# Kernel tuning notes

Hardware: AMD Instinct MI355X
Metric: run time of the kernel (lower is better)

## Reference

```python
import jax, jax.numpy as jnp
import numpy as np

D_MODEL = 1024
N_HEAD = 16
D_HEAD = D_MODEL // N_HEAD


def setup_inputs() -> dict:
    key = jax.random.key(0)
    k_x, k_qkv, k_proj = jax.random.split(key, 3)
    B, T = 2, 2048
    x = jax.random.normal(k_x, (B, T, D_MODEL), dtype=jnp.float32)
    # torch Linear weight [out, in]; y = x @ W.T. Scale ~ kaiming-uniform-ish.
    s = 1.0 / np.sqrt(D_MODEL)
    W_qkv = jax.random.uniform(k_qkv, (3 * D_MODEL, D_MODEL), dtype=jnp.float32, minval=-s, maxval=s)
    W_proj = jax.random.uniform(k_proj, (D_MODEL, D_MODEL), dtype=jnp.float32, minval=-s, maxval=s)
    return {"x": x, "W_qkv": W_qkv, "W_proj": W_proj}


def reference(x, W_qkv, W_proj):
    B, T, C = x.shape
    qkv = jnp.einsum('btc,oc->bto', x, W_qkv)  # [B,T,3C]
    q, k, v = jnp.split(qkv, 3, axis=-1)
    # [B,T,C] -> [B,H,T,Dh]
    def heads(t):
        return t.reshape(B, T, N_HEAD, D_HEAD).transpose(0, 2, 1, 3)
    q, k, v = heads(q), heads(k), heads(v)
    scale = 1.0 / np.sqrt(D_HEAD)
    scores = jnp.einsum('bhqd,bhkd->bhqk', q, k) * scale  # [B,H,T,T]
    causal = jnp.tril(jnp.ones((T, T), dtype=bool))
    scores = jnp.where(causal, scores, jnp.finfo(scores.dtype).min)
    attn = jax.nn.softmax(scores, axis=-1)
    y = jnp.einsum('bhqk,bhkd->bhqd', attn, v)  # [B,H,T,Dh]
    y = y.transpose(0, 2, 1, 3).reshape(B, T, C)
    return jnp.einsum('btc,oc->bto', y, W_proj)
```

## Files before the change

### kernel.cpp

```cpp
#include <hip/hip_runtime.h>

typedef unsigned short u16;
typedef float f32x4 __attribute__((ext_vector_type(4)));
typedef __bf16 bf16x8 __attribute__((ext_vector_type(8)));
typedef unsigned int u32x4 __attribute__((ext_vector_type(4)));
typedef u16 u16x4 __attribute__((ext_vector_type(4)));
typedef u16 u16x8 __attribute__((ext_vector_type(8)));

static __device__ __forceinline__ u16 f2bf(float f) {
  union { __bf16 h; u16 u; } c;
  c.h = (__bf16)f;
  return c.u;
}
static __device__ __forceinline__ float bf2f(u16 u) {
  union { unsigned u; float f; } c;
  c.u = ((unsigned)u) << 16;
  return c.f;
}

static __device__ __forceinline__ void gload_lds16(const void* g, void* l) {
  __builtin_amdgcn_global_load_lds(
      (const __attribute__((address_space(1))) unsigned int*)g,
      (__attribute__((address_space(3))) unsigned int*)l, 16, 0, 0);
}

__global__ __launch_bounds__(256) void cvt3_f32_bf16(const float* __restrict__ a,
                                                     const float* __restrict__ bb,
                                                     const float* __restrict__ cc,
                                                     u16* __restrict__ out,
                                                     int n1, int n2, int n3) {
  int i = blockIdx.x * 256 + threadIdx.x;
  const float* src;
  int j = i;
  if (i < n1) { src = a; }
  else if (i < n1 + n2) { src = bb; j = i - n1; }
  else { src = cc; j = i - n1 - n2; if (j >= n3) return; }
  f32x4 v = *((const f32x4*)src + j);
  u16x4 o;
  o[0] = f2bf(v[0]); o[1] = f2bf(v[1]); o[2] = f2bf(v[2]); o[3] = f2bf(v[3]);
  *((u16x4*)out + i) = o;
}

template<int OUT_BF16, int FUSE_VT>
__global__ __launch_bounds__(256) void gemm_nt(const u16* __restrict__ A,
                                               const u16* __restrict__ B,
                                               void* __restrict__ Cp,
                                               u16* __restrict__ vt,
                                               int M, int N, int K, int gy) {
  __shared__ __align__(16) u16 lA[128 * 64];
  __shared__ __align__(16) u16 lB[128 * 64];
  const int tid = threadIdx.x;
  const int lane = tid & 63;
  const int wave = tid >> 6;
  const int wm = wave >> 1, wn = wave & 1;
  const int l15 = lane & 15, lg = lane >> 4;

  const int bid = blockIdx.x;
  const int xcd = bid & 7, s = bid >> 3;
  const int pnx = (N >> 7) >> 3;
  const int bm = (s % gy) * 128;
  const int bn = (xcd * pnx + s / gy) * 128;

  f32x4 acc[4][4];
#pragma unroll
  for (int i = 0; i < 4; ++i)
#pragma unroll
    for (int j = 0; j < 4; ++j) acc[i][j] = (f32x4){0.f, 0.f, 0.f, 0.f};

  const u16* Ag[4];
  const u16* Bg[4];
#pragma unroll
  for (int it = 0; it < 4; ++it) {
    const int ss = it * 256 + tid;
    const int row = ss >> 3, g = ss & 7;
    const int gsw = g ^ (row & 7);
    Ag[it] = A + (size_t)(bm + row) * K + gsw * 8;
    Bg[it] = B + (size_t)(bn + row) * K + gsw * 8;
  }

  for (int k0 = 0; k0 < K; k0 += 64) {
#pragma unroll
    for (int it = 0; it < 4; ++it) {
      gload_lds16(Ag[it] + k0, (u16*)lA + (size_t)(it * 256 + tid) * 8);
      gload_lds16(Bg[it] + k0, (u16*)lB + (size_t)(it * 256 + tid) * 8);
    }
    __syncthreads();
#pragma unroll
    for (int kk = 0; kk < 2; ++kk) {
      bf16x8 af[4], bfv[4];
#pragma unroll
      for (int mf = 0; mf < 4; ++mf) {
        const int row = wm * 64 + mf * 16 + l15;
        af[mf] = *(const bf16x8*)((const char*)lA + row * 128 +
                                  ((kk * 64 + lg * 16) ^ ((row & 7) << 4)));
      }
#pragma unroll
      for (int nf = 0; nf < 4; ++nf) {
        const int row = wn * 64 + nf * 16 + l15;
        bfv[nf] = *(const bf16x8*)((const char*)lB + row * 128 +
                                   ((kk * 64 + lg * 16) ^ ((row & 7) << 4)));
      }
#pragma unroll
      for (int mf = 0; mf < 4; ++mf)
#pragma unroll
        for (int nf = 0; nf < 4; ++nf)
          acc[mf][nf] = __builtin_amdgcn_mfma_f32_16x16x32_bf16(af[mf], bfv[nf], acc[mf][nf], 0, 0, 0);
    }
    __syncthreads();
  }

  if (FUSE_VT && bn >= 2048) {
#pragma unroll
    for (int mf = 0; mf < 4; ++mf) {
      const int row0 = bm + wm * 64 + mf * 16 + lg * 4;
      const int b = row0 >> 11, t0 = row0 & 2047;
#pragma unroll
      for (int nf = 0; nf < 4; ++nf) {
        const int colv = bn - 2048 + wn * 64 + nf * 16 + l15;
        const int h = colv >> 6, d = colv & 63;
        u16x4 pk;
        pk[0] = f2bf(acc[mf][nf][0]); pk[1] = f2bf(acc[mf][nf][1]);
        pk[2] = f2bf(acc[mf][nf][2]); pk[3] = f2bf(acc[mf][nf][3]);
        *(u16x4*)&vt[((size_t)((b * 16 + h) * 64 + d)) * 2048 + t0] = pk;
      }
    }
  } else {
#pragma unroll
    for (int mf = 0; mf < 4; ++mf) {
#pragma unroll
      for (int r = 0; r < 4; ++r) {
        const int row = bm + wm * 64 + mf * 16 + lg * 4 + r;
#pragma unroll
        for (int nf = 0; nf < 4; ++nf) {
          const int col = bn + wn * 64 + nf * 16 + l15;
          const float v = acc[mf][nf][r];
          if (OUT_BF16) ((u16*)Cp)[(size_t)row * N + col] = f2bf(v);
          else          ((float*)Cp)[(size_t)row * N + col] = v;
        }
      }
    }
  }
}

__global__ __launch_bounds__(512) void attn_fwd(const u16* __restrict__ qkv,
                                                const u16* __restrict__ vt,
                                                u16* __restrict__ po,
                                                float* __restrict__ mlf) {
  constexpr int T = 2048, C = 1024, C3 = 3072, D = 64;
  __shared__ __align__(16) u16 lK[2][64 * 64];
  __shared__ __align__(16) u16 lV[2][64 * 64];
  __shared__ __align__(16) u16 lP[8 * 16 * 64];
  const int tid = threadIdx.x, lane = tid & 63, w = tid >> 6;
  const int l15 = lane & 15, lg = lane >> 4;

  const int bid = blockIdx.x;
  const int xcd = bid & 7, slot = bid >> 3;
  const int bh = xcd * 4 + (slot >> 4);
  const int rem = slot & 15;
  const int pi = rem >> 1, hf = rem & 1;
  const int b = bh >> 4, h = bh & 15;

  const int r0 = tid >> 3, off0 = (tid & 7) * 8;
  const int sb0 = (off0 * 2) ^ ((r0 & 7) << 4);
  const u16* Kbase = qkv + (size_t)b * T * C3 + C + h * D;
  const u16* Vbase = vt + (size_t)bh * D * T;
  char* lPb = (char*)lP + w * 2048;

  const float qscale = 0.125f * 1.44269504088896f;

#pragma unroll 1
  for (int qi = 0; qi < 2; ++qi) {
    const int qt = (qi == 0) ? pi : (15 - pi);
    const int q0 = qt * 128;
    const int kts = hf ? (qt + 1) : 0;
    const int kte = hf ? (2 * qt + 2) : (qt + 1);
    const int nit = kte - kts;
    const int qrow = q0 + w * 16 + l15;

    const size_t qoff = ((size_t)b * T + qrow) * C3 + h * D;
    const bf16x8 aq0 = *(const bf16x8*)&qkv[qoff + lg * 8];
    const bf16x8 aq1 = *(const bf16x8*)&qkv[qoff + 32 + lg * 8];

    float m = -1.0e30f, l = 0.f;
    f32x4 o_acc[4];
#pragma unroll
    for (int nf = 0; nf < 4; ++nf) o_acc[nf] = (f32x4){0.f, 0.f, 0.f, 0.f};

    u32x4 rk0 = *(const u32x4*)(Kbase + (size_t)(kts * 64 + r0) * C3 + off0);
    u32x4 rv0 = *(const u32x4*)(Vbase + (size_t)r0 * T + kts * 64 + off0);
    __syncthreads();
    *(u32x4*)&lK[0][(r0 * 128 + sb0) >> 1] = rk0;
    *(u32x4*)&lV[0][(r0 * 128 + sb0) >> 1] = rv0;
    if (nit > 1) {
      rk0 = *(const u32x4*)(Kbase + (size_t)((kts + 1) * 64 + r0) * C3 + off0);
      rv0 = *(const u32x4*)(Vbase + (size_t)r0 * T + (kts + 1) * 64 + off0);
    }

    for (int i = 0; i < nit; ++i) {
      const int kt = kts + i;
      const int cur = i & 1;
      __syncthreads();
      if (i < nit - 1) {
        *(u32x4*)&lK[cur ^ 1][(r0 * 128 + sb0) >> 1] = rk0;
        *(u32x4*)&lV[cur ^ 1][(r0 * 128 + sb0) >> 1] = rv0;
        if (i + 1 < nit - 1) {
          const int kn = (kt + 2) * 64;
          rk0 = *(const u32x4*)(Kbase + (size_t)(kn + r0) * C3 + off0);
          rv0 = *(const u32x4*)(Vbase + (size_t)r0 * T + kn + off0);
        }
      }
      const u16* Kc = lK[cur];
      const u16* Vc = lV[cur];

      f32x4 s[4];
#pragma unroll
      for (int nf = 0; nf < 4; ++nf) s[nf] = (f32x4){0.f, 0.f, 0.f, 0.f};
      __builtin_amdgcn_s_setprio(1);
#pragma unroll
      for (int nf = 0; nf < 4; ++nf) {
        const int row = nf * 16 + l15;
        const int x = (row & 7) << 4;
        bf16x8 bk0 = *(const bf16x8*)&Kc[(row * 128 + ((lg * 16) ^ x)) >> 1];
        bf16x8 bk1 = *(const bf16x8*)&Kc[(row * 128 + ((64 + lg * 16) ^ x)) >> 1];
        s[nf] = __builtin_amdgcn_mfma_f32_16x16x32_bf16(bk0, aq0, s[nf], 0, 0, 0);
        s[nf] = __builtin_amdgcn_mfma_f32_16x16x32_bf16(bk1, aq1, s[nf], 0, 0, 0);
      }
      __builtin_amdgcn_s_setprio(0);

      if (kt >= 2 * qt) {
        const int kb = kt * 64;
#pragma unroll
        for (int nf = 0; nf < 4; ++nf)
#pragma unroll
          for (int r = 0; r < 4; ++r) {
            float v = s[nf][r] * qscale;
            if (kb + nf * 16 + lg * 4 + r > qrow) v = -1.0e30f;
            s[nf][r] = v;
          }
      } else {
#pragma unroll
        for (int nf = 0; nf < 4; ++nf)
#pragma unroll
          for (int r = 0; r < 4; ++r) s[nf][r] *= qscale;
      }

      float t0a = fmaxf(fmaxf(s[0][0], s[0][1]), fmaxf(s[0][2], s[0][3]));
      float t1a = fmaxf(fmaxf(s[1][0], s[1][1]), fmaxf(s[1][2], s[1][3]));
      float t2a = fmaxf(fmaxf(s[2][0], s[2][1]), fmaxf(s[2][2], s[2][3]));
      float t3a = fmaxf(fmaxf(s[3][0], s[3][1]), fmaxf(s[3][2], s[3][3]));
      float pmax = fmaxf(fmaxf(t0a, t1a), fmaxf(t2a, t3a));
      pmax = fmaxf(pmax, __shfl_xor(pmax, 16));
      pmax = fmaxf(pmax, __shfl_xor(pmax, 32));

      if (!__all(pmax <= m)) {
        const float mnew = fmaxf(m, pmax);
        const float fct = __builtin_amdgcn_exp2f(m - mnew);
        m = mnew;
        l *= fct;
#pragma unroll
        for (int r = 0; r < 4; ++r) {
          const float fr = __shfl(fct, lg * 4 + r);
#pragma unroll
          for (int nf = 0; nf < 4; ++nf) o_acc[nf][r] *= fr;
        }
      }

      float p[4][4];
#pragma unroll
      for (int nf = 0; nf < 4; ++nf)
#pragma unroll
        for (int r = 0; r < 4; ++r) p[nf][r] = __builtin_amdgcn_exp2f(s[nf][r] - m);
      float s0a = (p[0][0] + p[0][1]) + (p[0][2] + p[0][3]);
      float s1a = (p[1][0] + p[1][1]) + (p[1][2] + p[1][3]);
      float s2a = (p[2][0] + p[2][1]) + (p[2][2] + p[2][3]);
      float s3a = (p[3][0] + p[3][1]) + (p[3][2] + p[3][3]);
      float psum = (s0a + s1a) + (s2a + s3a);
      psum += __shfl_xor(psum, 16);
      psum += __shfl_xor(psum, 32);
      l += psum;

#pragma unroll
      for (int nf = 0; nf < 4; ++nf) {
        u16x4 pk;
        pk[0] = f2bf(p[nf][0]); pk[1] = f2bf(p[nf][1]);
        pk[2] = f2bf(p[nf][2]); pk[3] = f2bf(p[nf][3]);
        *(u16x4*)(lPb + l15 * 128 + ((nf * 32 + lg * 8) ^ ((l15 & 7) << 4))) = pk;
      }

      __builtin_amdgcn_s_setprio(1);
#pragma unroll
      for (int sj = 0; sj < 2; ++sj) {
        bf16x8 ap = *(const bf16x8*)(lPb + l15 * 128 + ((sj * 64 + lg * 16) ^ ((l15 & 7) << 4)));
#pragma unroll
        for (int nf = 0; nf < 4; ++nf) {
          const int d = nf * 16 + l15;
          bf16x8 bv = *(const bf16x8*)&Vc[(d * 128 + ((sj * 64 + lg * 16) ^ ((d & 7) << 4))) >> 1];
          o_acc[nf] = __builtin_amdgcn_mfma_f32_16x16x32_bf16(ap, bv, o_acc[nf], 0, 0, 0);
        }
      }
      __builtin_amdgcn_s_setprio(0);
    }

    u16* pob = po + (size_t)hf * (4096ull * 1024ull);
#pragma unroll
    for (int r = 0; r < 4; ++r) {
      const float lv = __shfl(l, lg * 4 + r);
      const float li = (lv > 0.f) ? __builtin_amdgcn_rcpf(lv) : 0.f;
      const int row = q0 + w * 16 + lg * 4 + r;
#pragma unroll
      for (int nf = 0; nf < 4; ++nf) {
        const int col = h * D + nf * 16 + l15;
        pob[((size_t)b * T + row) * C + col] = f2bf(o_acc[nf][r] * li);
      }
    }
    if (lg == 0) {
      const size_t idx = (size_t)(b * T + qrow) * 16 + h;
      float* mp = mlf + (size_t)hf * 131072ull + idx * 2;
      mp[0] = m;
      mp[1] = l;
    }
  }
}

__global__ __launch_bounds__(256) void merge_o(const u16* __restrict__ po,
                                               const float* __restrict__ mlf,
                                               u16* __restrict__ y) {
  const int gid = blockIdx.x * 256 + threadIdx.x;
  const int row = gid >> 3, d0 = (gid & 7) * 8;
  const int bt = row >> 4, h = row & 15;
  const float m1 = mlf[row * 2], l1 = mlf[row * 2 + 1];
  const float m2 = mlf[131072 + row * 2], l2 = mlf[131072 + row * 2 + 1];
  const float ms = fmaxf(m1, m2);
  const float a1 = l1 * __builtin_amdgcn_exp2f(m1 - ms);
  const float a2 = l2 * __builtin_amdgcn_exp2f(m2 - ms);
  const float inv = __builtin_amdgcn_rcpf(a1 + a2);
  const float w1 = a1 * inv, w2 = a2 * inv;
  const size_t off = (size_t)bt * 1024 + h * 64 + d0;
  u16x8 p1 = *(const u16x8*)&po[off];
  u16x8 p2 = *(const u16x8*)&po[4194304ull + off];
  u16x8 o;
#pragma unroll
  for (int j = 0; j < 8; ++j) o[j] = f2bf(w1 * bf2f(p1[j]) + w2 * bf2f(p2[j]));
  *(u16x8*)&y[off] = o;
}

extern "C" void kernel_launch(void* const* d_in, const int* in_sizes, int n_in,
                              void* d_out, int out_size, void* d_ws, size_t ws_size,
                              hipStream_t stream) {
  const float* x = (const float*)d_in[0];
  const float* Wqkv = (const float*)d_in[1];
  const float* Wproj = (const float*)d_in[2];
  float* out = (float*)d_out;

  constexpr int B = 2, T = 2048, C = 1024, C3 = 3072, H = 16, D = 64;
  constexpr int M = B * T;

  u16* xb = (u16*)d_ws;
  u16* wqkvb = xb + (size_t)M * C;
  u16* wprojb = wqkvb + (size_t)C3 * C;
  u16* qkvb = wprojb + (size_t)C * C;
  u16* vtb = qkvb + (size_t)M * C3;
  u16* yb = vtb + (size_t)M * C;
  u16* po = yb + (size_t)M * C;
  float* mlf = (float*)(po + 2ull * M * C);

  constexpr int n1 = (M * C) / 4, n2 = (C3 * C) / 4, n3 = (C * C) / 4;
  cvt3_f32_bf16<<<dim3((n1 + n2 + n3 + 255) / 256), 256, 0, stream>>>(
      x, Wqkv, Wproj, xb, n1, n2, n3);

  gemm_nt<1, 1><<<dim3((C3 / 128) * (M / 128)), 256, 0, stream>>>(
      xb, wqkvb, qkvb, vtb, M, C3, C, M / 128);
  attn_fwd<<<dim3(512), 512, 0, stream>>>(qkvb, vtb, po, mlf);
  merge_o<<<dim3(2048), 256, 0, stream>>>(po, mlf, yb);
  gemm_nt<0, 0><<<dim3((C / 128) * (M / 128)), 256, 0, stream>>>(
      yb, wprojb, out, nullptr, M, C, C, M / 128);
}
```

Before: 110.8 us.

## Switch attention to 32x32 MFMA with register-resident P and three-way KV split

The attention kernel now uses 4 waves of 32 query rows each with 32x32x16 bf16 MFMA, keeping the softmax probabilities in registers. It packs them with v_cvt_pk_bf16_f32 and v_permlane32_swap instead of round-tripping P through LDS. The KV range is split three ways across 768 blocks instead of two, and a three-way merge kernel combines the partials, with the third partial buffer reusing the x bf16 workspace. Output is staged through LDS for 16-byte coalesced stores. The aim is to cut LDS traffic and shuffles and improve load balance and occupancy, at the cost of an extra partial buffer to write and read in the merge.

After: 266.2 us. +140.2%, slower.

```diff
diff --git a/kernel.cpp b/kernel.cpp
--- a/kernel.cpp
+++ b/kernel.cpp
@@ -2,6 +2,7 @@
 
 typedef unsigned short u16;
 typedef float f32x4 __attribute__((ext_vector_type(4)));
+typedef float f32x16 __attribute__((ext_vector_type(16)));
 typedef __bf16 bf16x8 __attribute__((ext_vector_type(8)));
 typedef unsigned int u32x4 __attribute__((ext_vector_type(4)));
 typedef u16 u16x4 __attribute__((ext_vector_type(4)));
@@ -16,6 +17,14 @@
   union { unsigned u; float f; } c;
   c.u = ((unsigned)u) << 16;
   return c.f;
+}
+static __device__ __forceinline__ unsigned cvtpk(float a, float b) {
+  unsigned r;
+  asm volatile("v_cvt_pk_bf16_f32 %0, %1, %2" : "=v"(r) : "v"(a), "v"(b));
+  return r;
+}
+static __device__ __forceinline__ void plswap(unsigned& a, unsigned& b) {
+  asm volatile("v_permlane32_swap_b32 %0, %1" : "+v"(a), "+v"(b));
 }
 
 static __device__ __forceinline__ void gload_lds16(const void* g, void* l) {
@@ -142,29 +151,32 @@
   }
 }
 
-__global__ __launch_bounds__(512) void attn_fwd(const u16* __restrict__ qkv,
-                                                const u16* __restrict__ vt,
-                                                u16* __restrict__ po,
-                                                float* __restrict__ mlf) {
-  constexpr int T = 2048, C = 1024, C3 = 3072, D = 64;
+__global__ __launch_bounds__(256, 3) void attn_fwd(const u16* __restrict__ qkv,
+                                                   const u16* __restrict__ vt,
+                                                   u16* __restrict__ po0,
+                                                   u16* __restrict__ po1,
+                                                   u16* __restrict__ po2,
+                                                   float* __restrict__ mlf) {
+  constexpr int T = 2048, C3 = 3072;
   __shared__ __align__(16) u16 lK[2][64 * 64];
   __shared__ __align__(16) u16 lV[2][64 * 64];
-  __shared__ __align__(16) u16 lP[8 * 16 * 64];
   const int tid = threadIdx.x, lane = tid & 63, w = tid >> 6;
-  const int l15 = lane & 15, lg = lane >> 4;
+  const int l31 = lane & 31, h5 = lane >> 5;
 
   const int bid = blockIdx.x;
   const int xcd = bid & 7, slot = bid >> 3;
-  const int bh = xcd * 4 + (slot >> 4);
-  const int rem = slot & 15;
-  const int pi = rem >> 1, hf = rem & 1;
+  const int bh = xcd * 4 + slot / 24;
+  const int rem = slot % 24;
+  const int pi = rem / 3, tr = rem % 3;
   const int b = bh >> 4, h = bh & 15;
 
   const int r0 = tid >> 3, off0 = (tid & 7) * 8;
+  const int r1 = r0 + 32;
   const int sb0 = (off0 * 2) ^ ((r0 & 7) << 4);
-  const u16* Kbase = qkv + (size_t)b * T * C3 + C + h * D;
-  const u16* Vbase = vt + (size_t)bh * D * T;
-  char* lPb = (char*)lP + w * 2048;
+  const int sb1 = (off0 * 2) ^ ((r1 & 7) << 4);
+  const u16* Kbase = qkv + (size_t)b * T * C3 + 1024 + h * 64;
+  const u16* Vbase = vt + (size_t)bh * 64 * T;
+  u16* pob = (tr == 0) ? po0 : ((tr == 1) ? po1 : po2);
 
   const float qscale = 0.125f * 1.44269504088896f;
 
@@ -172,175 +184,216 @@
   for (int qi = 0; qi < 2; ++qi) {
     const int qt = (qi == 0) ? pi : (15 - pi);
     const int q0 = qt * 128;
-    const int kts = hf ? (qt + 1) : 0;
-    const int kte = hf ? (2 * qt + 2) : (qt + 1);
+    const int n = 2 * qt + 2;
+    const int kts = tr * n / 3, kte = (tr + 1) * n / 3;
     const int nit = kte - kts;
-    const int qrow = q0 + w * 16 + l15;
-
-    const size_t qoff = ((size_t)b * T + qrow) * C3 + h * D;
-    const bf16x8 aq0 = *(const bf16x8*)&qkv[qoff + lg * 8];
-    const bf16x8 aq1 = *(const bf16x8*)&qkv[qoff + 32 + lg * 8];
+    const int qrow = q0 + w * 32 + l31;
+
+    const size_t qoff = ((size_t)b * T + qrow) * C3 + h * 64;
+    bf16x8 aq[4];
+#pragma unroll
+    for (int ks = 0; ks < 4; ++ks)
+      aq[ks] = *(const bf16x8*)&qkv[qoff + ks * 16 + h5 * 8];
 
     float m = -1.0e30f, l = 0.f;
-    f32x4 o_acc[4];
-#pragma unroll
-    for (int nf = 0; nf < 4; ++nf) o_acc[nf] = (f32x4){0.f, 0.f, 0.f, 0.f};
-
-    u32x4 rk0 = *(const u32x4*)(Kbase + (size_t)(kts * 64 + r0) * C3 + off0);
-    u32x4 rv0 = *(const u32x4*)(Vbase + (size_t)r0 * T + kts * 64 + off0);
+    f32x16 o0, o1;
+#pragma unroll
+    for (int r = 0; r < 16; ++r) { o0[r] = 0.f; o1[r] = 0.f; }
+
+    if (nit > 0) {
+      u32x4 rk0 = *(const u32x4*)(Kbase + (size_t)(kts * 64 + r0) * C3 + off0);
+      u32x4 rk1 = *(const u32x4*)(Kbase + (size_t)(kts * 64 + r1) * C3 + off0);
+      u32x4 rv0 = *(const u32x4*)(Vbase + (size_t)r0 * T + kts * 64 + off0);
+      u32x4 rv1 = *(const u32x4*)(Vbase + (size_t)r1 * T + kts * 64 + off0);
+      __syncthreads();
+      *(u32x4*)((char*)lK[0] + r0 * 128 + sb0) = rk0;
+      *(u32x4*)((char*)lK[0] + r1 * 128 + sb1) = rk1;
+      *(u32x4*)((char*)lV[0] + r0 * 128 + sb0) = rv0;
+      *(u32x4*)((char*)lV[0] + r1 * 128 + sb1) = rv1;
+      if (nit > 1) {
+        rk0 = *(const u32x4*)(Kbase + (size_t)((kts + 1) * 64 + r0) * C3 + off0);
+        rk1 = *(const u32x4*)(Kbase + (size_t)((kts + 1) * 64 + r1) * C3 + off0);
+        rv0 = *(const u32x4*)(Vbase + (size_t)r0 * T + (kts + 1) * 64 + off0);
+        rv1 = *(const u32x4*)(Vbase + (size_t)r1 * T + (kts + 1) * 64 + off0);
+      }
+
+      for (int i = 0; i < nit; ++i) {
+        const int kt = kts + i;
+        const int cur = i & 1;
+        __syncthreads();
+        if (i < nit - 1) {
+          *(u32x4*)((char*)lK[cur ^ 1] + r0 * 128 + sb0) = rk0;
+          *(u32x4*)((char*)lK[cur ^ 1] + r1 * 128 + sb1) = rk1;
+          *(u32x4*)((char*)lV[cur ^ 1] + r0 * 128 + sb0) = rv0;
+          *(u32x4*)((char*)lV[cur ^ 1] + r1 * 128 + sb1) = rv1;
+          if (i + 1 < nit - 1) {
+            const int kn = (kt + 2) * 64;
+            rk0 = *(const u32x4*)(Kbase + (size_t)(kn + r0) * C3 + off0);
+            rk1 = *(const u32x4*)(Kbase + (size_t)(kn + r1) * C3 + off0);
+            rv0 = *(const u32x4*)(Vbase + (size_t)r0 * T + kn + off0);
+            rv1 = *(const u32x4*)(Vbase + (size_t)r1 * T + kn + off0);
+          }
+        }
+        const char* Kc = (const char*)lK[cur];
+        const char* Vc = (const char*)lV[cur];
+
+        f32x16 s0, s1;
+#pragma unroll
+        for (int r = 0; r < 16; ++r) { s0[r] = 0.f; s1[r] = 0.f; }
+        __builtin_amdgcn_s_setprio(1);
+#pragma unroll
+        for (int ks = 0; ks < 4; ++ks) {
+          const int cb = (ks * 32 + h5 * 16);
+          bf16x8 kf0 = *(const bf16x8*)(Kc + l31 * 128 + (cb ^ ((l31 & 7) << 4)));
+          bf16x8 kf1 = *(const bf16x8*)(Kc + (32 + l31) * 128 + (cb ^ ((l31 & 7) << 4)));
+          s0 = __builtin_amdgcn_mfma_f32_32x32x16_bf16(kf0, aq[ks], s0, 0, 0, 0);
+          s1 = __builtin_amdgcn_mfma_f32_32x32x16_bf16(kf1, aq[ks], s1, 0, 0, 0);
+        }
+        __builtin_amdgcn_s_setprio(0);
+
+        if (kt >= 2 * qt) {
+          const int kb0 = kt * 64;
+#pragma unroll
+          for (int r = 0; r < 16; ++r) {
+            const int kvl = (r & 3) + 8 * (r >> 2) + 4 * h5;
+            float v0 = s0[r] * qscale;
+            float v1 = s1[r] * qscale;
+            if (kb0 + kvl > qrow) v0 = -1.0e30f;
+            if (kb0 + 32 + kvl > qrow) v1 = -1.0e30f;
+            s0[r] = v0; s1[r] = v1;
+          }
+        } else {
+#pragma unroll
+          for (int r = 0; r < 16; ++r) { s0[r] *= qscale; s1[r] *= qscale; }
+        }
+
+        float t0 = fmaxf(fmaxf(s0[0], s0[1]), fmaxf(s0[2], s0[3]));
+        float t1 = fmaxf(fmaxf(s0[4], s0[5]), fmaxf(s0[6], s0[7]));
+        float t2 = fmaxf(fmaxf(s0[8], s0[9]), fmaxf(s0[10], s0[11]));
+        float t3 = fmaxf(fmaxf(s0[12], s0[13]), fmaxf(s0[14], s0[15]));
+        float t4 = fmaxf(fmaxf(s1[0], s1[1]), fmaxf(s1[2], s1[3]));
+        float t5 = fmaxf(fmaxf(s1[4], s1[5]), fmaxf(s1[6], s1[7]));
+        float t6 = fmaxf(fmaxf(s1[8], s1[9]), fmaxf(s1[10], s1[11]));
+        float t7 = fmaxf(fmaxf(s1[12], s1[13]), fmaxf(s1[14], s1[15]));
+        float pmax = fmaxf(fmaxf(fmaxf(t0, t1), fmaxf(t2, t3)),
+                           fmaxf(fmaxf(t4, t5), fmaxf(t6, t7)));
+        pmax = fmaxf(pmax, __shfl_xor(pmax, 32));
+
+        if (!__all(pmax <= m)) {
+          const float mnew = fmaxf(m, pmax);
+          const float fct = __builtin_amdgcn_exp2f(m - mnew);
+          m = mnew;
+          l *= fct;
+#pragma unroll
+          for (int r = 0; r < 16; ++r) { o0[r] *= fct; o1[r] *= fct; }
+        }
+
+#pragma unroll
+        for (int r = 0; r < 16; ++r) {
+          s0[r] = __builtin_amdgcn_exp2f(s0[r] - m);
+          s1[r] = __builtin_amdgcn_exp2f(s1[r] - m);
+        }
+        float u0 = (s0[0] + s0[1]) + (s0[2] + s0[3]);
+        float u1 = (s0[4] + s0[5]) + (s0[6] + s0[7]);
+        float u2 = (s0[8] + s0[9]) + (s0[10] + s0[11]);
+        float u3 = (s0[12] + s0[13]) + (s0[14] + s0[15]);
+        float u4 = (s1[0] + s1[1]) + (s1[2] + s1[3]);
+        float u5 = (s1[4] + s1[5]) + (s1[6] + s1[7]);
+        float u6 = (s1[8] + s1[9]) + (s1[10] + s1[11]);
+        float u7 = (s1[12] + s1[13]) + (s1[14] + s1[15]);
+        float psum = ((u0 + u1) + (u2 + u3)) + ((u4 + u5) + (u6 + u7));
+        psum += __shfl_xor(psum, 32);
+        l += psum;
+
+        union { u32x4 u; bf16x8 b; } pb[4];
+        {
+          unsigned A = cvtpk(s0[0], s0[1]), Bw = cvtpk(s0[2], s0[3]);
+          unsigned Cw = cvtpk(s0[4], s0[5]), Dw = cvtpk(s0[6], s0[7]);
+          unsigned E = cvtpk(s0[8], s0[9]), F = cvtpk(s0[10], s0[11]);
+          unsigned G = cvtpk(s0[12], s0[13]), H = cvtpk(s0[14], s0[15]);
+          plswap(A, Cw); plswap(Bw, Dw); plswap(E, G); plswap(F, H);
+          pb[0].u = (u32x4){A, Bw, Cw, Dw};
+          pb[1].u = (u32x4){E, F, G, H};
+        }
+        {
+          unsigned A = cvtpk(s1[0], s1[1]), Bw = cvtpk(s1[2], s1[3]);
+          unsigned Cw = cvtpk(s1[4], s1[5]), Dw = cvtpk(s1[6], s1[7]);
+          unsigned E = cvtpk(s1[8], s1[9]), F = cvtpk(s1[10], s1[11]);
+          unsigned G = cvtpk(s1[12], s1[13]), H = cvtpk(s1[14], s1[15]);
+          plswap(A, Cw); plswap(Bw, Dw); plswap(E, G); plswap(F, H);
+          pb[2].u = (u32x4){A, Bw, Cw, Dw};
+          pb[3].u = (u32x4){E, F, G, H};
+        }
+
+        __builtin_amdgcn_s_setprio(1);
+#pragma unroll
+        for (int kk = 0; kk < 4; ++kk) {
+          const int cb = (kk * 32 + h5 * 16);
+          bf16x8 vf0 = *(const bf16x8*)(Vc + l31 * 128 + (cb ^ ((l31 & 7) << 4)));
+          bf16x8 vf1 = *(const bf16x8*)(Vc + (32 + l31) * 128 + (cb ^ ((l31 & 7) << 4)));
+          o0 = __builtin_amdgcn_mfma_f32_32x32x16_bf16(vf0, pb[kk].b, o0, 0, 0, 0);
+          o1 = __builtin_amdgcn_mfma_f32_32x32x16_bf16(vf1, pb[kk].b, o1, 0, 0, 0);
+        }
+        __builtin_amdgcn_s_setprio(0);
+      }
+    }
+
     __syncthreads();
-    *(u32x4*)&lK[0][(r0 * 128 + sb0) >> 1] = rk0;
-    *(u32x4*)&lV[0][(r0 * 128 + sb0) >> 1] = rv0;
-    if (nit > 1) {
-      rk0 = *(const u32x4*)(Kbase + (size_t)((kts + 1) * 64 + r0) * C3 + off0);
-      rv0 = *(const u32x4*)(Vbase + (size_t)r0 * T + (kts + 1) * 64 + off0);
-    }
-
-    for (int i = 0; i < nit; ++i) {
-      const int kt = kts + i;
-      const int cur = i & 1;
-      __syncthreads();
-      if (i < nit - 1) {
-        *(u32x4*)&lK[cur ^ 1][(r0 * 128 + sb0) >> 1] = rk0;
-        *(u32x4*)&lV[cur ^ 1][(r0 * 128 + sb0) >> 1] = rv0;
-        if (i + 1 < nit - 1) {
-          const int kn = (kt + 2) * 64;
-          rk0 = *(const u32x4*)(Kbase + (size_t)(kn + r0) * C3 + off0);
-          rv0 = *(const u32x4*)(Vbase + (size_t)r0 * T + kn + off0);
-        }
-      }
-      const u16* Kc = lK[cur];
-      const u16* Vc = lV[cur];
-
-      f32x4 s[4];
-#pragma unroll
-      for (int nf = 0; nf < 4; ++nf) s[nf] = (f32x4){0.f, 0.f, 0.f, 0.f};
-      __builtin_amdgcn_s_setprio(1);
-#pragma unroll
-      for (int nf = 0; nf < 4; ++nf) {
-        const int row = nf * 16 + l15;
-        const int x = (row & 7) << 4;
-        bf16x8 bk0 = *(const bf16x8*)&Kc[(row * 128 + ((lg * 16) ^ x)) >> 1];
-        bf16x8 bk1 = *(const bf16x8*)&Kc[(row * 128 + ((64 + lg * 16) ^ x)) >> 1];
-        s[nf] = __builtin_amdgcn_mfma_f32_16x16x32_bf16(bk0, aq0, s[nf], 0, 0, 0);
-        s[nf] = __builtin_amdgcn_mfma_f32_16x16x32_bf16(bk1, aq1, s[nf], 0, 0, 0);
-      }
-      __builtin_amdgcn_s_setprio(0);
-
-      if (kt >= 2 * qt) {
-        const int kb = kt * 64;
-#pragma unroll
-        for (int nf = 0; nf < 4; ++nf)
-#pragma unroll
-          for (int r = 0; r < 4; ++r) {
-            float v = s[nf][r] * qscale;
-            if (kb + nf * 16 + lg * 4 + r > qrow) v = -1.0e30f;
-            s[nf][r] = v;
-          }
-      } else {
-#pragma unroll
-        for (int nf = 0; nf < 4; ++nf)
-#pragma unroll
-          for (int r = 0; r < 4; ++r) s[nf][r] *= qscale;
-      }
-
-      float t0a = fmaxf(fmaxf(s[0][0], s[0][1]), fmaxf(s[0][2], s[0][3]));
-      float t1a = fmaxf(fmaxf(s[1][0], s[1][1]), fmaxf(s[1][2], s[1][3]));
-      float t2a = fmaxf(fmaxf(s[2][0], s[2][1]), fmaxf(s[2][2], s[2][3]));
-      float t3a = fmaxf(fmaxf(s[3][0], s[3][1]), fmaxf(s[3][2], s[3][3]));
-      float pmax = fmaxf(fmaxf(t0a, t1a), fmaxf(t2a, t3a));
-      pmax = fmaxf(pmax, __shfl_xor(pmax, 16));
-      pmax = fmaxf(pmax, __shfl_xor(pmax, 32));
-
-      if (!__all(pmax <= m)) {
-        const float mnew = fmaxf(m, pmax);
-        const float fct = __builtin_amdgcn_exp2f(m - mnew);
-        m = mnew;
-        l *= fct;
-#pragma unroll
-        for (int r = 0; r < 4; ++r) {
-          const float fr = __shfl(fct, lg * 4 + r);
-#pragma unroll
-          for (int nf = 0; nf < 4; ++nf) o_acc[nf][r] *= fr;
-        }
-      }
-
-      float p[4][4];
-#pragma unroll
-      for (int nf = 0; nf < 4; ++nf)
-#pragma unroll
-        for (int r = 0; r < 4; ++r) p[nf][r] = __builtin_amdgcn_exp2f(s[nf][r] - m);
-      float s0a = (p[0][0] + p[0][1]) + (p[0][2] + p[0][3]);
-      float s1a = (p[1][0] + p[1][1]) + (p[1][2] + p[1][3]);
-      float s2a = (p[2][0] + p[2][1]) + (p[2][2] + p[2][3]);
-      float s3a = (p[3][0] + p[3][1]) + (p[3][2] + p[3][3]);
-      float psum = (s0a + s1a) + (s2a + s3a);
-      psum += __shfl_xor(psum, 16);
-      psum += __shfl_xor(psum, 32);
-      l += psum;
-
-#pragma unroll
-      for (int nf = 0; nf < 4; ++nf) {
-        u16x4 pk;
-        pk[0] = f2bf(p[nf][0]); pk[1] = f2bf(p[nf][1]);
-        pk[2] = f2bf(p[nf][2]); pk[3] = f2bf(p[nf][3]);
-        *(u16x4*)(lPb + l15 * 128 + ((nf * 32 + lg * 8) ^ ((l15 & 7) << 4))) = pk;
-      }
-
-      __builtin_amdgcn_s_setprio(1);
-#pragma unroll
-      for (int sj = 0; sj < 2; ++sj) {
-        bf16x8 ap = *(const bf16x8*)(lPb + l15 * 128 + ((sj * 64 + lg * 16) ^ ((l15 & 7) << 4)));
-#pragma unroll
-        for (int nf = 0; nf < 4; ++nf) {
-          const int d = nf * 16 + l15;
-          bf16x8 bv = *(const bf16x8*)&Vc[(d * 128 + ((sj * 64 + lg * 16) ^ ((d & 7) << 4))) >> 1];
-          o_acc[nf] = __builtin_amdgcn_mfma_f32_16x16x32_bf16(ap, bv, o_acc[nf], 0, 0, 0);
-        }
-      }
-      __builtin_amdgcn_s_setprio(0);
-    }
-
-    u16* pob = po + (size_t)hf * (4096ull * 1024ull);
-#pragma unroll
-    for (int r = 0; r < 4; ++r) {
-      const float lv = __shfl(l, lg * 4 + r);
-      const float li = (lv > 0.f) ? __builtin_amdgcn_rcpf(lv) : 0.f;
-      const int row = q0 + w * 16 + lg * 4 + r;
-#pragma unroll
-      for (int nf = 0; nf < 4; ++nf) {
-        const int col = h * D + nf * 16 + l15;
-        pob[((size_t)b * T + row) * C + col] = f2bf(o_acc[nf][r] * li);
-      }
-    }
-    if (lg == 0) {
-      const size_t idx = (size_t)(b * T + qrow) * 16 + h;
-      float* mp = mlf + (size_t)hf * 131072ull + idx * 2;
+    const float li = (l > 0.f) ? __builtin_amdgcn_rcpf(l) : 0.f;
+    char* bnc = (char*)lK + w * 4096;
+#pragma unroll
+    for (int db = 0; db < 2; ++db) {
+#pragma unroll
+      for (int rg = 0; rg < 4; ++rg) {
+        u16x4 pk4;
+        if (db == 0) {
+          pk4[0] = f2bf(o0[rg * 4 + 0] * li); pk4[1] = f2bf(o0[rg * 4 + 1] * li);
+          pk4[2] = f2bf(o0[rg * 4 + 2] * li); pk4[3] = f2bf(o0[rg * 4 + 3] * li);
+        } else {
+          pk4[0] = f2bf(o1[rg * 4 + 0] * li); pk4[1] = f2bf(o1[rg * 4 + 1] * li);
+          pk4[2] = f2bf(o1[rg * 4 + 2] * li); pk4[3] = f2bf(o1[rg * 4 + 3] * li);
+        }
+        *(u16x4*)(bnc + l31 * 128 + db * 64 + rg * 16 + h5 * 8) = pk4;
+      }
+    }
+#pragma unroll
+    for (int j = 0; j < 4; ++j) {
+      u16x8 vv = *(const u16x8*)(bnc + l31 * 128 + h5 * 64 + j * 16);
+      *(u16x8*)&pob[((size_t)b * T + q0 + w * 32 + l31) * 1024 + h * 64 + h5 * 32 + j * 8] = vv;
+    }
+    if (h5 == 0) {
+      float* mp = mlf + (size_t)tr * 131072ull + ((size_t)(b * T + qrow) * 16 + h) * 2;
       mp[0] = m;
       mp[1] = l;
     }
   }
 }
 
-__global__ __launch_bounds__(256) void merge_o(const u16* __restrict__ po,
-                                               const float* __restrict__ mlf,
-                                               u16* __restrict__ y) {
+__global__ __launch_bounds__(256) void merge3(const u16* __restrict__ p0,
+                                              const u16* __restrict__ p1,
+                                              const u16* __restrict__ p2,
+                                              const float* __restrict__ mlf,
+                                              u16* __restrict__ y) {
   const int gid = blockIdx.x * 256 + threadIdx.x;
   const int row = gid >> 3, d0 = (gid & 7) * 8;
-  const int bt = row >> 4, h = row & 15;
+  const int bt = row >> 4, hh = row & 15;
   const float m1 = mlf[row * 2], l1 = mlf[row * 2 + 1];
   const float m2 = mlf[131072 + row * 2], l2 = mlf[131072 + row * 2 + 1];
-  const float ms = fmaxf(m1, m2);
+  const float m3 = mlf[262144 + row * 2], l3 = mlf[262144 + row * 2 + 1];
+  const float ms = fmaxf(fmaxf(m1, m2), m3);
   const float a1 = l1 * __builtin_amdgcn_exp2f(m1 - ms);
   const float a2 = l2 * __builtin_amdgcn_exp2f(m2 - ms);
-  const float inv = __builtin_amdgcn_rcpf(a1 + a2);
-  const float w1 = a1 * inv, w2 = a2 * inv;
-  const size_t off = (size_t)bt * 1024 + h * 64 + d0;
-  u16x8 p1 = *(const u16x8*)&po[off];
-  u16x8 p2 = *(const u16x8*)&po[4194304ull + off];
+  const float a3 = l3 * __builtin_amdgcn_exp2f(m3 - ms);
+  const float inv = __builtin_amdgcn_rcpf(a1 + a2 + a3);
+  const float w1 = a1 * inv, w2 = a2 * inv, w3 = a3 * inv;
+  const size_t off = (size_t)bt * 1024 + hh * 64 + d0;
+  u16x8 q1 = *(const u16x8*)&p0[off];
+  u16x8 q2 = *(const u16x8*)&p1[off];
+  u16x8 q3 = *(const u16x8*)&p2[off];
   u16x8 o;
 #pragma unroll
-  for (int j = 0; j < 8; ++j) o[j] = f2bf(w1 * bf2f(p1[j]) + w2 * bf2f(p2[j]));
+  for (int j = 0; j < 8; ++j)
+    o[j] = f2bf(w1 * bf2f(q1[j]) + w2 * bf2f(q2[j]) + w3 * bf2f(q3[j]));
   *(u16x8*)&y[off] = o;
 }
 
@@ -363,6 +416,7 @@
   u16* yb = vtb + (size_t)M * C;
   u16* po = yb + (size_t)M * C;
   float* mlf = (float*)(po + 2ull * M * C);
+  u16* po2 = xb;
 
   constexpr int n1 = (M * C) / 4, n2 = (C3 * C) / 4, n3 = (C * C) / 4;
   cvt3_f32_bf16<<<dim3((n1 + n2 + n3 + 255) / 256), 256, 0, stream>>>(
@@ -370,8 +424,8 @@
 
   gemm_nt<1, 1><<<dim3((C3 / 128) * (M / 128)), 256, 0, stream>>>(
       xb, wqkvb, qkvb, vtb, M, C3, C, M / 128);
-  attn_fwd<<<dim3(512), 512, 0, stream>>>(qkvb, vtb, po, mlf);
-  merge_o<<<dim3(2048), 256, 0, stream>>>(po, mlf, yb);
+  attn_fwd<<<dim3(768), 256, 0, stream>>>(qkvb, vtb, po, po + (size_t)M * C, po2, mlf);
+  merge3<<<dim3(2048), 256, 0, stream>>>(po, po + (size_t)M * C, po2, mlf, yb);
   gemm_nt<0, 0><<<dim3((C / 128) * (M / 128)), 256, 0, stream>>>(
       yb, wprojb, out, nullptr, M, C, C, M / 128);
 }
```

## Split causal attention key range three ways and merge three partials

Applied to the files above, without the earlier changes.

The attention kernel now splits each query tile's causal key range into three segments instead of two. That raises the grid from 512 to 768 blocks, shortens per-block work and should fill more slots per CU. The merge kernel combines three partial outputs using their (m, l) statistics. The third partial buffer reuses the bf16 x workspace, which is dead after the QKV GEMM. In exchange the code adds an extra partial write and read plus a third mlf slice, and some segments can be empty for short rows.

Measured after the change: 120.5 us. +8.7%, slower.

```diff
diff --git a/kernel.cpp b/kernel.cpp
--- a/kernel.cpp
+++ b/kernel.cpp
@@ -144,9 +144,11 @@
 
 __global__ __launch_bounds__(512) void attn_fwd(const u16* __restrict__ qkv,
                                                 const u16* __restrict__ vt,
-                                                u16* __restrict__ po,
+                                                u16* __restrict__ po0,
+                                                u16* __restrict__ po1,
+                                                u16* __restrict__ po2,
                                                 float* __restrict__ mlf) {
-  constexpr int T = 2048, C = 1024, C3 = 3072, D = 64;
+  constexpr int T = 2048, C = 1024, C3 = 3072;
   __shared__ __align__(16) u16 lK[2][64 * 64];
   __shared__ __align__(16) u16 lV[2][64 * 64];
   __shared__ __align__(16) u16 lP[8 * 16 * 64];
@@ -155,16 +157,17 @@
 
   const int bid = blockIdx.x;
   const int xcd = bid & 7, slot = bid >> 3;
-  const int bh = xcd * 4 + (slot >> 4);
-  const int rem = slot & 15;
-  const int pi = rem >> 1, hf = rem & 1;
+  const int bh = xcd * 4 + slot / 24;
+  const int rem = slot % 24;
+  const int pi = rem / 3, tr = rem % 3;
   const int b = bh >> 4, h = bh & 15;
 
   const int r0 = tid >> 3, off0 = (tid & 7) * 8;
   const int sb0 = (off0 * 2) ^ ((r0 & 7) << 4);
-  const u16* Kbase = qkv + (size_t)b * T * C3 + C + h * D;
-  const u16* Vbase = vt + (size_t)bh * D * T;
+  const u16* Kbase = qkv + (size_t)b * T * C3 + C + h * 64;
+  const u16* Vbase = vt + (size_t)bh * 64 * T;
   char* lPb = (char*)lP + w * 2048;
+  u16* pob = (tr == 0) ? po0 : ((tr == 1) ? po1 : po2);
 
   const float qscale = 0.125f * 1.44269504088896f;
 
@@ -172,12 +175,13 @@
   for (int qi = 0; qi < 2; ++qi) {
     const int qt = (qi == 0) ? pi : (15 - pi);
     const int q0 = qt * 128;
-    const int kts = hf ? (qt + 1) : 0;
-    const int kte = hf ? (2 * qt + 2) : (qt + 1);
+    const int nkt = 2 * qt + 2;
+    const int kts = tr * nkt / 3;
+    const int kte = (tr + 1) * nkt / 3;
     const int nit = kte - kts;
     const int qrow = q0 + w * 16 + l15;
 
-    const size_t qoff = ((size_t)b * T + qrow) * C3 + h * D;
+    const size_t qoff = ((size_t)b * T + qrow) * C3 + h * 64;
     const bf16x8 aq0 = *(const bf16x8*)&qkv[qoff + lg * 8];
     const bf16x8 aq1 = *(const bf16x8*)&qkv[qoff + 32 + lg * 8];
 
@@ -186,122 +190,123 @@
 #pragma unroll
     for (int nf = 0; nf < 4; ++nf) o_acc[nf] = (f32x4){0.f, 0.f, 0.f, 0.f};
 
-    u32x4 rk0 = *(const u32x4*)(Kbase + (size_t)(kts * 64 + r0) * C3 + off0);
-    u32x4 rv0 = *(const u32x4*)(Vbase + (size_t)r0 * T + kts * 64 + off0);
-    __syncthreads();
-    *(u32x4*)&lK[0][(r0 * 128 + sb0) >> 1] = rk0;
-    *(u32x4*)&lV[0][(r0 * 128 + sb0) >> 1] = rv0;
-    if (nit > 1) {
-      rk0 = *(const u32x4*)(Kbase + (size_t)((kts + 1) * 64 + r0) * C3 + off0);
-      rv0 = *(const u32x4*)(Vbase + (size_t)r0 * T + (kts + 1) * 64 + off0);
-    }
-
-    for (int i = 0; i < nit; ++i) {
-      const int kt = kts + i;
-      const int cur = i & 1;
+    if (nit > 0) {
+      u32x4 rk0 = *(const u32x4*)(Kbase + (size_t)(kts * 64 + r0) * C3 + off0);
+      u32x4 rv0 = *(const u32x4*)(Vbase + (size_t)r0 * T + kts * 64 + off0);
       __syncthreads();
-      if (i < nit - 1) {
-        *(u32x4*)&lK[cur ^ 1][(r0 * 128 + sb0) >> 1] = rk0;
-        *(u32x4*)&lV[cur ^ 1][(r0 * 128 + sb0) >> 1] = rv0;
-        if (i + 1 < nit - 1) {
-          const int kn = (kt + 2) * 64;
-          rk0 = *(const u32x4*)(Kbase + (size_t)(kn + r0) * C3 + off0);
-          rv0 = *(const u32x4*)(Vbase + (size_t)r0 * T + kn + off0);
-        }
-      }
-      const u16* Kc = lK[cur];
-      const u16* Vc = lV[cur];
-
-      f32x4 s[4];
-#pragma unroll
-      for (int nf = 0; nf < 4; ++nf) s[nf] = (f32x4){0.f, 0.f, 0.f, 0.f};
-      __builtin_amdgcn_s_setprio(1);
-#pragma unroll
-      for (int nf = 0; nf < 4; ++nf) {
-        const int row = nf * 16 + l15;
-        const int x = (row & 7) << 4;
-        bf16x8 bk0 = *(const bf16x8*)&Kc[(row * 128 + ((lg * 16) ^ x)) >> 1];
-        bf16x8 bk1 = *(const bf16x8*)&Kc[(row * 128 + ((64 + lg * 16) ^ x)) >> 1];
-        s[nf] = __builtin_amdgcn_mfma_f32_16x16x32_bf16(bk0, aq0, s[nf], 0, 0, 0);
-        s[nf] = __builtin_amdgcn_mfma_f32_16x16x32_bf16(bk1, aq1, s[nf], 0, 0, 0);
-      }
-      __builtin_amdgcn_s_setprio(0);
-
-      if (kt >= 2 * qt) {
-        const int kb = kt * 64;
+      *(u32x4*)&lK[0][(r0 * 128 + sb0) >> 1] = rk0;
+      *(u32x4*)&lV[0][(r0 * 128 + sb0) >> 1] = rv0;
+      if (nit > 1) {
+        rk0 = *(const u32x4*)(Kbase + (size_t)((kts + 1) * 64 + r0) * C3 + off0);
+        rv0 = *(const u32x4*)(Vbase + (size_t)r0 * T + (kts + 1) * 64 + off0);
+      }
+
+      for (int i = 0; i < nit; ++i) {
+        const int kt = kts + i;
+        const int cur = i & 1;
+        __syncthreads();
+        if (i < nit - 1) {
+          *(u32x4*)&lK[cur ^ 1][(r0 * 128 + sb0) >> 1] = rk0;
+          *(u32x4*)&lV[cur ^ 1][(r0 * 128 + sb0) >> 1] = rv0;
+          if (i + 1 < nit - 1) {
+            const int kn = (kt + 2) * 64;
+            rk0 = *(const u32x4*)(Kbase + (size_t)(kn + r0) * C3 + off0);
+            rv0 = *(const u32x4*)(Vbase + (size_t)r0 * T + kn + off0);
+          }
+        }
+        const u16* Kc = lK[cur];
+        const u16* Vc = lV[cur];
+
+        f32x4 s[4];
+#pragma unroll
+        for (int nf = 0; nf < 4; ++nf) s[nf] = (f32x4){0.f, 0.f, 0.f, 0.f};
+        __builtin_amdgcn_s_setprio(1);
+#pragma unroll
+        for (int nf = 0; nf < 4; ++nf) {
+          const int row = nf * 16 + l15;
+          const int x = (row & 7) << 4;
+          bf16x8 bk0 = *(const bf16x8*)&Kc[(row * 128 + ((lg * 16) ^ x)) >> 1];
+          bf16x8 bk1 = *(const bf16x8*)&Kc[(row * 128 + ((64 + lg * 16) ^ x)) >> 1];
+          s[nf] = __builtin_amdgcn_mfma_f32_16x16x32_bf16(bk0, aq0, s[nf], 0, 0, 0);
+          s[nf] = __builtin_amdgcn_mfma_f32_16x16x32_bf16(bk1, aq1, s[nf], 0, 0, 0);
+        }
+        __builtin_amdgcn_s_setprio(0);
+
+        if (kt >= 2 * qt) {
+          const int kb = kt * 64;
+#pragma unroll
+          for (int nf = 0; nf < 4; ++nf)
+#pragma unroll
+            for (int r = 0; r < 4; ++r) {
+              float v = s[nf][r] * qscale;
+              if (kb + nf * 16 + lg * 4 + r > qrow) v = -1.0e30f;
+              s[nf][r] = v;
+            }
+        } else {
+#pragma unroll
+          for (int nf = 0; nf < 4; ++nf)
+#pragma unroll
+            for (int r = 0; r < 4; ++r) s[nf][r] *= qscale;
+        }
+
+        float t0a = fmaxf(fmaxf(s[0][0], s[0][1]), fmaxf(s[0][2], s[0][3]));
+        float t1a = fmaxf(fmaxf(s[1][0], s[1][1]), fmaxf(s[1][2], s[1][3]));
+        float t2a = fmaxf(fmaxf(s[2][0], s[2][1]), fmaxf(s[2][2], s[2][3]));
+        float t3a = fmaxf(fmaxf(s[3][0], s[3][1]), fmaxf(s[3][2], s[3][3]));
+        float pmax = fmaxf(fmaxf(t0a, t1a), fmaxf(t2a, t3a));
+        pmax = fmaxf(pmax, __shfl_xor(pmax, 16));
+        pmax = fmaxf(pmax, __shfl_xor(pmax, 32));
+
+        if (!__all(pmax <= m)) {
+          const float mnew = fmaxf(m, pmax);
+          const float fct = __builtin_amdgcn_exp2f(m - mnew);
+          m = mnew;
+          l *= fct;
+#pragma unroll
+          for (int r = 0; r < 4; ++r) {
+            const float fr = __shfl(fct, lg * 4 + r);
+#pragma unroll
+            for (int nf = 0; nf < 4; ++nf) o_acc[nf][r] *= fr;
+          }
+        }
+
+        float p[4][4];
 #pragma unroll
         for (int nf = 0; nf < 4; ++nf)
 #pragma unroll
-          for (int r = 0; r < 4; ++r) {
-            float v = s[nf][r] * qscale;
-            if (kb + nf * 16 + lg * 4 + r > qrow) v = -1.0e30f;
-            s[nf][r] = v;
+          for (int r = 0; r < 4; ++r) p[nf][r] = __builtin_amdgcn_exp2f(s[nf][r] - m);
+        float s0a = (p[0][0] + p[0][1]) + (p[0][2] + p[0][3]);
+        float s1a = (p[1][0] + p[1][1]) + (p[1][2] + p[1][3]);
+        float s2a = (p[2][0] + p[2][1]) + (p[2][2] + p[2][3]);
+        float s3a = (p[3][0] + p[3][1]) + (p[3][2] + p[3][3]);
+        float psum = (s0a + s1a) + (s2a + s3a);
+        psum += __shfl_xor(psum, 16);
+        psum += __shfl_xor(psum, 32);
+        l += psum;
+
+#pragma unroll
+        for (int nf = 0; nf < 4; ++nf) {
+          u16x4 pk;
+          pk[0] = f2bf(p[nf][0]); pk[1] = f2bf(p[nf][1]);
+          pk[2] = f2bf(p[nf][2]); pk[3] = f2bf(p[nf][3]);
+          *(u16x4*)(lPb + l15 * 128 + ((nf * 32 + lg * 8) ^ ((l15 & 7) << 4))) = pk;
+        }
+
+        __builtin_amdgcn_s_setprio(1);
+#pragma unroll
+        for (int sj = 0; sj < 2; ++sj) {
+          bf16x8 ap = *(const bf16x8*)(lPb + l15 * 128 + ((sj * 64 + lg * 16) ^ ((l15 & 7) << 4)));
+#pragma unroll
+          for (int nf = 0; nf < 4; ++nf) {
+            const int d = nf * 16 + l15;
+            bf16x8 bv = *(const bf16x8*)&Vc[(d * 128 + ((sj * 64 + lg * 16) ^ ((d & 7) << 4))) >> 1];
+            o_acc[nf] = __builtin_amdgcn_mfma_f32_16x16x32_bf16(ap, bv, o_acc[nf], 0, 0, 0);
           }
-      } else {
-#pragma unroll
-        for (int nf = 0; nf < 4; ++nf)
-#pragma unroll
-          for (int r = 0; r < 4; ++r) s[nf][r] *= qscale;
-      }
-
-      float t0a = fmaxf(fmaxf(s[0][0], s[0][1]), fmaxf(s[0][2], s[0][3]));
-      float t1a = fmaxf(fmaxf(s[1][0], s[1][1]), fmaxf(s[1][2], s[1][3]));
-      float t2a = fmaxf(fmaxf(s[2][0], s[2][1]), fmaxf(s[2][2], s[2][3]));
-      float t3a = fmaxf(fmaxf(s[3][0], s[3][1]), fmaxf(s[3][2], s[3][3]));
-      float pmax = fmaxf(fmaxf(t0a, t1a), fmaxf(t2a, t3a));
-      pmax = fmaxf(pmax, __shfl_xor(pmax, 16));
-      pmax = fmaxf(pmax, __shfl_xor(pmax, 32));
-
-      if (!__all(pmax <= m)) {
-        const float mnew = fmaxf(m, pmax);
-        const float fct = __builtin_amdgcn_exp2f(m - mnew);
-        m = mnew;
-        l *= fct;
-#pragma unroll
-        for (int r = 0; r < 4; ++r) {
-          const float fr = __shfl(fct, lg * 4 + r);
-#pragma unroll
-          for (int nf = 0; nf < 4; ++nf) o_acc[nf][r] *= fr;
-        }
-      }
-
-      float p[4][4];
-#pragma unroll
-      for (int nf = 0; nf < 4; ++nf)
-#pragma unroll
-        for (int r = 0; r < 4; ++r) p[nf][r] = __builtin_amdgcn_exp2f(s[nf][r] - m);
-      float s0a = (p[0][0] + p[0][1]) + (p[0][2] + p[0][3]);
-      float s1a = (p[1][0] + p[1][1]) + (p[1][2] + p[1][3]);
-      float s2a = (p[2][0] + p[2][1]) + (p[2][2] + p[2][3]);
-      float s3a = (p[3][0] + p[3][1]) + (p[3][2] + p[3][3]);
-      float psum = (s0a + s1a) + (s2a + s3a);
-      psum += __shfl_xor(psum, 16);
-      psum += __shfl_xor(psum, 32);
-      l += psum;
-
-#pragma unroll
-      for (int nf = 0; nf < 4; ++nf) {
-        u16x4 pk;
-        pk[0] = f2bf(p[nf][0]); pk[1] = f2bf(p[nf][1]);
-        pk[2] = f2bf(p[nf][2]); pk[3] = f2bf(p[nf][3]);
-        *(u16x4*)(lPb + l15 * 128 + ((nf * 32 + lg * 8) ^ ((l15 & 7) << 4))) = pk;
-      }
-
-      __builtin_amdgcn_s_setprio(1);
-#pragma unroll
-      for (int sj = 0; sj < 2; ++sj) {
-        bf16x8 ap = *(const bf16x8*)(lPb + l15 * 128 + ((sj * 64 + lg * 16) ^ ((l15 & 7) << 4)));
-#pragma unroll
-        for (int nf = 0; nf < 4; ++nf) {
-          const int d = nf * 16 + l15;
-          bf16x8 bv = *(const bf16x8*)&Vc[(d * 128 + ((sj * 64 + lg * 16) ^ ((d & 7) << 4))) >> 1];
-          o_acc[nf] = __builtin_amdgcn_mfma_f32_16x16x32_bf16(ap, bv, o_acc[nf], 0, 0, 0);
-        }
-      }
-      __builtin_amdgcn_s_setprio(0);
-    }
-
-    u16* pob = po + (size_t)hf * (4096ull * 1024ull);
+        }
+        __builtin_amdgcn_s_setprio(0);
+      }
+    }
+
 #pragma unroll
     for (int r = 0; r < 4; ++r) {
       const float lv = __shfl(l, lg * 4 + r);
@@ -309,38 +314,43 @@
       const int row = q0 + w * 16 + lg * 4 + r;
 #pragma unroll
       for (int nf = 0; nf < 4; ++nf) {
-        const int col = h * D + nf * 16 + l15;
+        const int col = h * 64 + nf * 16 + l15;
         pob[((size_t)b * T + row) * C + col] = f2bf(o_acc[nf][r] * li);
       }
     }
     if (lg == 0) {
-      const size_t idx = (size_t)(b * T + qrow) * 16 + h;
-      float* mp = mlf + (size_t)hf * 131072ull + idx * 2;
+      float* mp = mlf + (size_t)tr * 131072ull + ((size_t)(b * T + qrow) * 16 + h) * 2;
       mp[0] = m;
       mp[1] = l;
     }
   }
 }
 
-__global__ __launch_bounds__(256) void merge_o(const u16* __restrict__ po,
-                                               const float* __restrict__ mlf,
-                                               u16* __restrict__ y) {
+__global__ __launch_bounds__(256) void merge3(const u16* __restrict__ p0,
+                                              const u16* __restrict__ p1,
+                                              const u16* __restrict__ p2,
+                                              const float* __restrict__ mlf,
+                                              u16* __restrict__ y) {
   const int gid = blockIdx.x * 256 + threadIdx.x;
   const int row = gid >> 3, d0 = (gid & 7) * 8;
-  const int bt = row >> 4, h = row & 15;
+  const int bt = row >> 4, hh = row & 15;
   const float m1 = mlf[row * 2], l1 = mlf[row * 2 + 1];
   const float m2 = mlf[131072 + row * 2], l2 = mlf[131072 + row * 2 + 1];
-  const float ms = fmaxf(m1, m2);
+  const float m3 = mlf[262144 + row * 2], l3 = mlf[262144 + row * 2 + 1];
+  const float ms = fmaxf(fmaxf(m1, m2), m3);
   const float a1 = l1 * __builtin_amdgcn_exp2f(m1 - ms);
   const float a2 = l2 * __builtin_amdgcn_exp2f(m2 - ms);
-  const float inv = __builtin_amdgcn_rcpf(a1 + a2);
-  const float w1 = a1 * inv, w2 = a2 * inv;
-  const size_t off = (size_t)bt * 1024 + h * 64 + d0;
-  u16x8 p1 = *(const u16x8*)&po[off];
-  u16x8 p2 = *(const u16x8*)&po[4194304ull + off];
+  const float a3 = l3 * __builtin_amdgcn_exp2f(m3 - ms);
+  const float inv = __builtin_amdgcn_rcpf(a1 + a2 + a3);
+  const float w1 = a1 * inv, w2 = a2 * inv, w3 = a3 * inv;
+  const size_t off = (size_t)bt * 1024 + hh * 64 + d0;
+  u16x8 q1 = *(const u16x8*)&p0[off];
+  u16x8 q2 = *(const u16x8*)&p1[off];
+  u16x8 q3 = *(const u16x8*)&p2[off];
   u16x8 o;
 #pragma unroll
-  for (int j = 0; j < 8; ++j) o[j] = f2bf(w1 * bf2f(p1[j]) + w2 * bf2f(p2[j]));
+  for (int j = 0; j < 8; ++j)
+    o[j] = f2bf(w1 * bf2f(q1[j]) + w2 * bf2f(q2[j]) + w3 * bf2f(q3[j]));
   *(u16x8*)&y[off] = o;
 }
 
@@ -363,6 +373,7 @@
   u16* yb = vtb + (size_t)M * C;
   u16* po = yb + (size_t)M * C;
   float* mlf = (float*)(po + 2ull * M * C);
+  u16* po2 = xb;
 
   constexpr int n1 = (M * C) / 4, n2 = (C3 * C) / 4, n3 = (C * C) / 4;
   cvt3_f32_bf16<<<dim3((n1 + n2 + n3 + 255) / 256), 256, 0, stream>>>(
@@ -370,8 +381,8 @@
 
   gemm_nt<1, 1><<<dim3((C3 / 128) * (M / 128)), 256, 0, stream>>>(
       xb, wqkvb, qkvb, vtb, M, C3, C, M / 128);
-  attn_fwd<<<dim3(512), 512, 0, stream>>>(qkvb, vtb, po, mlf);
-  merge_o<<<dim3(2048), 256, 0, stream>>>(po, mlf, yb);
+  attn_fwd<<<dim3(768), 512, 0, stream>>>(qkvb, vtb, po, po + (size_t)M * C, po2, mlf);
+  merge3<<<dim3(2048), 256, 0, stream>>>(po, po + (size_t)M * C, po2, mlf, yb);
   gemm_nt<0, 0><<<dim3((C / 128) * (M / 128)), 256, 0, stream>>>(
       yb, wprojb, out, nullptr, M, C, C, M / 128);
 }
```
